# Performance work log

Measured on AMD Instinct MI355X. Metric: run time of the kernel, lower is better.

Reference implementation:

```python
import jax, jax.numpy as jnp
import numpy as np

TRANSFER_VOLUME = 0.1
KW = 1e-14  # water ion product
LN10 = float(np.log(10.0))


def binarize_weight(w):
    # clip to [-1,1], forward pass is sign(), gradient flows through the clip (STE)
    clipped = jnp.clip(w, -1.0, 1.0)
    rounded = jnp.sign(clipped)
    return clipped + jax.lax.stop_gradient(rounded - clipped)


def setup_inputs() -> dict:
    key = jax.random.key(0)
    kx, kw = jax.random.split(key)
    batch, n_in, n_out = 4096, 4096, 4096
    x = jax.random.uniform(kx, (batch, n_in), dtype=jnp.float32)
    w = jax.random.normal(kw, (n_in, n_out), dtype=jnp.float32)
    return {"x": x, "w": w}


def reference(x, w):
    binary_weights = binarize_weight(w)  # [n_in, n_out], values in {-1, 0, +1}
    input_sz = x.shape[1]
    input_h_conc = 10.0 ** (-x)                       # [B, n_in]
    input_oh_conc = KW / input_h_conc                  # [B, n_in]
    input_h_num_moles = input_h_conc * TRANSFER_VOLUME
    input_oh_num_moles = input_oh_conc * TRANSFER_VOLUME
    acid_moles_sum = input_h_num_moles @ binary_weights   # [B, n_out]
    base_moles_sum = input_oh_num_moles @ binary_weights  # [B, n_out]
    remaining_moles = acid_moles_sum - base_moles_sum
    acid_is_limiting = remaining_moles < 0
    remaining_moles_conc = jnp.abs(remaining_moles) / (input_sz * TRANSFER_VOLUME)
    resultant_h_conc = jnp.where(acid_is_limiting, KW / remaining_moles_conc, remaining_moles_conc)
    resultant_ph = -jnp.log(resultant_h_conc) / LN10
    return resultant_ph
```

## Files before the change

kernel.cpp:

```cpp
#include <hip/hip_runtime.h>
#include <math.h>

#define BATCH 4096
#define NIN   4096
#define NOUT  4096

#define BM 128
#define BN 64
#define BK 32
#define NSTAGE (NIN / BK)

typedef __attribute__((ext_vector_type(8))) short bf16x8;
typedef __attribute__((ext_vector_type(4))) float f32x4;
typedef __attribute__((ext_vector_type(8))) unsigned short u16x8;

__device__ __forceinline__ float2 compute_terms(float xv) {
    float h  = (float)exp10(-(double)xv);
    float oh = 1e-14f / h;
    return make_float2(h * 0.1f, oh * 0.1f);
}

__device__ __forceinline__ unsigned short bf16_rne(float v) {
    unsigned int b = __float_as_uint(v);
    return (unsigned short)((b + 0x7FFFu + ((b >> 16) & 1u)) >> 16);
}

__global__ __launch_bounds__(256) void precompute_terms2(const float* __restrict__ x,
                                                         float* __restrict__ a_acid,
                                                         unsigned short* __restrict__ a_b16,
                                                         int n) {
    int stride = gridDim.x * blockDim.x;
    for (int i = blockIdx.x * blockDim.x + threadIdx.x; i < n; i += stride) {
        float2 t = compute_terms(x[i]);
        a_acid[i] = t.x;
        a_b16[i]  = bf16_rne(t.y);
    }
}

__device__ __forceinline__ float signf_of(float wv) {
    return (wv > 0.f) ? 1.f : ((wv < 0.f) ? -1.f : 0.f);
}
__device__ __forceinline__ unsigned short signbf16_of(float wv) {
    return (wv > 0.f) ? 0x3F80u : ((wv < 0.f) ? 0xBF80u : 0u);
}

#define OFF_BS    16896
#define OFF_BA    25600
#define OFF_BT    35840

__global__ __launch_bounds__(256, 2) void acid_gemm_hyb(const float* __restrict__ Aa,
                                                        const unsigned short* __restrict__ Ab,
                                                        const float* __restrict__ W,
                                                        float* __restrict__ out) {
    __shared__ __align__(16) char smem[40960];
    float*          As_acid = (float*)smem;
    float*          Bs      = (float*)(smem + OFF_BS);
    unsigned short* baseA   = (unsigned short*)(smem + OFF_BA);
    unsigned short* Bt      = (unsigned short*)(smem + OFF_BT);
    float*          Bout    = (float*)smem;

    const int tid  = threadIdx.x;
    const int tx   = tid & 15;
    const int ty   = tid >> 4;
    const int lane = tid & 63;
    const int wv   = tid >> 6;
    const int g    = lane >> 4;
    const int r16  = lane & 15;
    const int bm0  = blockIdx.y * BM;
    const int bn0  = blockIdx.x * BN;

    float ma[8][4] = {}, ca[8][4] = {};
    f32x4 acc[2][4] = {};

    float4 areg[4];
    bf16x8 breg[2];
    float4 wreg[2];

    #define ISSUE_LOADS(s)                                                         \
        {                                                                          \
            const int k0_ = (s) * BK;                                              \
            _Pragma("unroll")                                                      \
            for (int r = 0; r < 4; ++r)                                            \
                areg[r] = *(const float4*)(Aa +                                    \
                    (size_t)(bm0 + (tid >> 3) + 32 * r) * NIN + k0_ + (tid & 7) * 4);\
            _Pragma("unroll")                                                      \
            for (int r = 0; r < 2; ++r)                                            \
                breg[r] = *(const bf16x8*)(Ab +                                    \
                    (size_t)(bm0 + (tid >> 2) + 64 * r) * NIN + k0_ + (tid & 3) * 8);\
            _Pragma("unroll")                                                      \
            for (int r = 0; r < 2; ++r)                                            \
                wreg[r] = *(const float4*)(W +                                     \
                    (size_t)(k0_ + (tid >> 4) + 16 * r) * NOUT + bn0 + (tid & 15) * 4);\
        }

    #define WRITE_LDS()                                                            \
        {                                                                          \
            _Pragma("unroll")                                                      \
            for (int r = 0; r < 4; ++r) {                                          \
                int m_ = (tid >> 3) + 32 * r, q_ = (tid & 7) * 4;                  \
                As_acid[(q_ + 0) * 132 + m_] = areg[r].x;                          \
                As_acid[(q_ + 1) * 132 + m_] = areg[r].y;                          \
                As_acid[(q_ + 2) * 132 + m_] = areg[r].z;                          \
                As_acid[(q_ + 3) * 132 + m_] = areg[r].w;                          \
            }                                                                      \
            _Pragma("unroll")                                                      \
            for (int r = 0; r < 2; ++r)                                            \
                *(bf16x8*)&baseA[((tid >> 2) + 64 * r) * 40 + (tid & 3) * 8] = breg[r];\
            _Pragma("unroll")                                                      \
            for (int r = 0; r < 2; ++r) {                                          \
                float4 w_ = wreg[r];                                               \
                *(float4*)&Bs[((tid >> 4) + 16 * r) * 68 + (tid & 15) * 4] =       \
                    make_float4(signf_of(w_.x), signf_of(w_.y),                    \
                                signf_of(w_.z), signf_of(w_.w));                   \
                int kk_ = (tid >> 4) + 16 * r;                                     \
                Bt[((tid & 15) * 4 + 0) * 40 + kk_] = signbf16_of(w_.x);           \
                Bt[((tid & 15) * 4 + 1) * 40 + kk_] = signbf16_of(w_.y);           \
                Bt[((tid & 15) * 4 + 2) * 40 + kk_] = signbf16_of(w_.z);           \
                Bt[((tid & 15) * 4 + 3) * 40 + kk_] = signbf16_of(w_.w);           \
            }                                                                      \
        }

    ISSUE_LOADS(0);
    WRITE_LDS();
    __syncthreads();

    for (int s = 0; s < NSTAGE; ++s) {
        if (s + 1 < NSTAGE) ISSUE_LOADS(s + 1);

        {
            bf16x8 af0 = *(const bf16x8*)&baseA[(wv * 32 +      r16) * 40 + g * 8];
            bf16x8 af1 = *(const bf16x8*)&baseA[(wv * 32 + 16 + r16) * 40 + g * 8];
            #pragma unroll
            for (int tc = 0; tc < 4; ++tc) {
                bf16x8 bf = *(const bf16x8*)&Bt[(tc * 16 + r16) * 40 + g * 8];
                acc[0][tc] = __builtin_amdgcn_mfma_f32_16x16x32_bf16(af0, bf, acc[0][tc], 0, 0, 0);
                acc[1][tc] = __builtin_amdgcn_mfma_f32_16x16x32_bf16(af1, bf, acc[1][tc], 0, 0, 0);
            }
        }

        #pragma unroll 8
        for (int k = 0; k < BK; ++k) {
            const float4 pa = *(const float4*)&As_acid[k * 132 + ty * 8];
            const float4 pb = *(const float4*)&As_acid[k * 132 + ty * 8 + 4];
            const float4 sv = *(const float4*)&Bs[k * 68 + tx * 4];
            const float av[8] = {pa.x, pa.y, pa.z, pa.w, pb.x, pb.y, pb.z, pb.w};
            const float sn[4] = {sv.x, sv.y, sv.z, sv.w};
            #pragma unroll
            for (int m = 0; m < 8; ++m)
                #pragma unroll
                for (int n = 0; n < 4; ++n)
                    ca[m][n] = fmaf(av[m], sn[n], ca[m][n]);
        }

        if (((s + 1) & 15) == 0) {
            #pragma unroll
            for (int m = 0; m < 8; ++m)
                #pragma unroll
                for (int n = 0; n < 4; ++n) {
                    ma[m][n] += ca[m][n]; ca[m][n] = 0.f;
                }
        }

        __syncthreads();
        if (s + 1 < NSTAGE) WRITE_LDS();
        __syncthreads();
    }

    #pragma unroll
    for (int tr = 0; tr < 2; ++tr)
        #pragma unroll
        for (int tc = 0; tc < 4; ++tc)
            #pragma unroll
            for (int rr = 0; rr < 4; ++rr)
                Bout[(wv * 32 + tr * 16 + g * 4 + rr) * 68 + tc * 16 + r16] = acc[tr][tc][rr];
    __syncthreads();

    #pragma unroll
    for (int m = 0; m < 8; ++m) {
        int row = ty * 8 + m;
        const float4 bv = *(const float4*)&Bout[row * 68 + tx * 4];
        const float bb[4] = {bv.x, bv.y, bv.z, bv.w};
        #pragma unroll
        for (int n = 0; n < 4; ++n) {
            float r    = ma[m][n] - bb[n];
            float conc = fabsf(r) / 409.6f;
            float hc   = (r < 0.f) ? (1e-14f / conc) : conc;
            float ph   = (-logf(hc)) / 2.302585092994046f;
            out[(size_t)(bm0 + row) * NOUT + bn0 + tx * 4 + n] = ph;
        }
    }
    #undef ISSUE_LOADS
    #undef WRITE_LDS
}

__global__ __launch_bounds__(256, 2) void acid_gemm_fly(const float* __restrict__ X,
                                                        const float* __restrict__ W,
                                                        float* __restrict__ out) {
    __shared__ float2 Asf[BK][BM + 2];
    __shared__ float  Bsf[BK][BN];
    const int tid = threadIdx.x;
    const int tx = tid & 15, ty = tid >> 4;
    const int bm0 = blockIdx.y * BM, bn0 = blockIdx.x * BN;
    float ma[8][4] = {}, mb[8][4] = {}, ca[8][4] = {}, cb[8][4] = {};
    for (int s = 0; s < NSTAGE; ++s) {
        const int k0 = s * BK;
        for (int idx = tid; idx < BM * BK; idx += 256) {
            int m = idx >> 5, k = idx & 31;
            Asf[k][m] = compute_terms(X[(size_t)(bm0 + m) * NIN + k0 + k]);
        }
        for (int idx = tid; idx < BK * BN; idx += 256) {
            int k = idx >> 6, c = idx & 63;
            Bsf[k][c] = signf_of(W[(size_t)(k0 + k) * NOUT + bn0 + c]);
        }
        __syncthreads();
        #pragma unroll 4
        for (int k = 0; k < BK; ++k) {
            float2 av[8]; float sv[4];
            #pragma unroll
            for (int m = 0; m < 8; ++m) av[m] = Asf[k][ty * 8 + m];
            #pragma unroll
            for (int n = 0; n < 4; ++n) sv[n] = Bsf[k][tx * 4 + n];
            #pragma unroll
            for (int m = 0; m < 8; ++m)
                #pragma unroll
                for (int n = 0; n < 4; ++n) {
                    ca[m][n] = fmaf(av[m].x, sv[n], ca[m][n]);
                    cb[m][n] = fmaf(av[m].y, sv[n], cb[m][n]);
                }
        }
        if (((s + 1) & 15) == 0) {
            #pragma unroll
            for (int m = 0; m < 8; ++m)
                #pragma unroll
                for (int n = 0; n < 4; ++n) {
                    ma[m][n] += ca[m][n]; ca[m][n] = 0.f;
                    mb[m][n] += cb[m][n]; cb[m][n] = 0.f;
                }
        }
        __syncthreads();
    }
    #pragma unroll
    for (int m = 0; m < 8; ++m) {
        int row = bm0 + ty * 8 + m;
        #pragma unroll
        for (int n = 0; n < 4; ++n) {
            int col = bn0 + tx * 4 + n;
            float r = ma[m][n] - mb[m][n];
            float conc = fabsf(r) / 409.6f;
            float hc = (r < 0.f) ? (1e-14f / conc) : conc;
            out[(size_t)row * NOUT + col] = (-logf(hc)) / 2.302585092994046f;
        }
    }
}

extern "C" void kernel_launch(void* const* d_in, const int* in_sizes, int n_in,
                              void* d_out, int out_size, void* d_ws, size_t ws_size,
                              hipStream_t stream) {
    const float* x = (const float*)d_in[0];
    const float* w = (const float*)d_in[1];
    float* out = (float*)d_out;

    const size_t nElem   = (size_t)BATCH * NIN;
    const size_t needWs  = nElem * 4 + nElem * 2;
    dim3 grid(NOUT / BN, BATCH / BM);

    if (ws_size >= needWs) {
        float*          a_acid = (float*)d_ws;
        unsigned short* a_b16  = (unsigned short*)((char*)d_ws + nElem * 4);
        precompute_terms2<<<4096, 256, 0, stream>>>(x, a_acid, a_b16, (int)nElem);
        acid_gemm_hyb<<<grid, dim3(256), 0, stream>>>(a_acid, a_b16, w, out);
    } else {
        acid_gemm_fly<<<grid, dim3(256), 0, stream>>>(x, w, out);
    }
}
```

Before: 2.242 ms.

## Pre-transpose acid operand and weight signs to vectorize LDS staging

The acid terms are now written by the precompute kernel in k-major (transposed) layout, and a new precompute kernel builds a transposed bf16 sign matrix of the weights. The GEMM can then store both into shared memory with vector writes instead of scattered scalar transposing stores. This removes per-tile LDS transpose work and bank-conflicting scalar stores inside the main loop. In exchange it adds an extra kernel, an extra 32 MB workspace buffer and more global reads per stage.

Measured after the change: 2.489 ms. +11.0%, slower.

```diff
diff --git a/kernel.cpp b/kernel.cpp
--- a/kernel.cpp
+++ b/kernel.cpp
@@ -11,32 +11,18 @@
 #define NSTAGE (NIN / BK)
 
 typedef __attribute__((ext_vector_type(8))) short bf16x8;
+typedef __attribute__((ext_vector_type(8))) unsigned short u16x8;
 typedef __attribute__((ext_vector_type(4))) float f32x4;
-typedef __attribute__((ext_vector_type(8))) unsigned short u16x8;
 
 __device__ __forceinline__ float2 compute_terms(float xv) {
     float h  = (float)exp10(-(double)xv);
     float oh = 1e-14f / h;
     return make_float2(h * 0.1f, oh * 0.1f);
 }
-
 __device__ __forceinline__ unsigned short bf16_rne(float v) {
     unsigned int b = __float_as_uint(v);
     return (unsigned short)((b + 0x7FFFu + ((b >> 16) & 1u)) >> 16);
 }
-
-__global__ __launch_bounds__(256) void precompute_terms2(const float* __restrict__ x,
-                                                         float* __restrict__ a_acid,
-                                                         unsigned short* __restrict__ a_b16,
-                                                         int n) {
-    int stride = gridDim.x * blockDim.x;
-    for (int i = blockIdx.x * blockDim.x + threadIdx.x; i < n; i += stride) {
-        float2 t = compute_terms(x[i]);
-        a_acid[i] = t.x;
-        a_b16[i]  = bf16_rne(t.y);
-    }
-}
-
 __device__ __forceinline__ float signf_of(float wv) {
     return (wv > 0.f) ? 1.f : ((wv < 0.f) ? -1.f : 0.f);
 }
@@ -44,12 +30,67 @@
     return (wv > 0.f) ? 0x3F80u : ((wv < 0.f) ? 0xBF80u : 0u);
 }
 
-#define OFF_BS    16896
-#define OFF_BA    25600
-#define OFF_BT    35840
-
-__global__ __launch_bounds__(256, 2) void acid_gemm_hyb(const float* __restrict__ Aa,
+__global__ __launch_bounds__(256) void precompute_A(const float* __restrict__ x,
+                                                    float* __restrict__ aaT,
+                                                    unsigned short* __restrict__ ab) {
+    __shared__ float tile[64][65];
+    const int m0 = blockIdx.y * 64, k0 = blockIdx.x * 64;
+    const int tid = threadIdx.x;
+    #pragma unroll
+    for (int it = 0; it < 4; ++it) {
+        int idx = tid + it * 256;
+        int row = idx >> 4, q = idx & 15;
+        float4 xv = *(const float4*)(x + (size_t)(m0 + row) * NIN + k0 + q * 4);
+        float2 t0 = compute_terms(xv.x), t1 = compute_terms(xv.y),
+               t2 = compute_terms(xv.z), t3 = compute_terms(xv.w);
+        *(ushort4*)(ab + (size_t)(m0 + row) * NIN + k0 + q * 4) =
+            make_ushort4(bf16_rne(t0.y), bf16_rne(t1.y), bf16_rne(t2.y), bf16_rne(t3.y));
+        tile[row][q * 4 + 0] = t0.x; tile[row][q * 4 + 1] = t1.x;
+        tile[row][q * 4 + 2] = t2.x; tile[row][q * 4 + 3] = t3.x;
+    }
+    __syncthreads();
+    #pragma unroll
+    for (int it = 0; it < 4; ++it) {
+        int idx = tid + it * 256;
+        int krow = idx >> 4, q = idx & 15;
+        float4 v = make_float4(tile[q * 4 + 0][krow], tile[q * 4 + 1][krow],
+                               tile[q * 4 + 2][krow], tile[q * 4 + 3][krow]);
+        *(float4*)(aaT + (size_t)(k0 + krow) * NIN + m0 + q * 4) = v;
+    }
+}
+
+__global__ __launch_bounds__(256) void precompute_signT(const float* __restrict__ w,
+                                                        unsigned short* __restrict__ sT) {
+    __shared__ unsigned short tile[64][68];
+    const int k0 = blockIdx.y * 64, n0 = blockIdx.x * 64;
+    const int tid = threadIdx.x;
+    #pragma unroll
+    for (int it = 0; it < 4; ++it) {
+        int idx = tid + it * 256;
+        int krow = idx >> 4, q = idx & 15;
+        float4 wv = *(const float4*)(w + (size_t)(k0 + krow) * NOUT + n0 + q * 4);
+        *(ushort4*)&tile[krow][q * 4] =
+            make_ushort4(signbf16_of(wv.x), signbf16_of(wv.y), signbf16_of(wv.z), signbf16_of(wv.w));
+    }
+    __syncthreads();
+    #pragma unroll
+    for (int it = 0; it < 2; ++it) {
+        int idx = tid + it * 256;
+        int n = idx >> 3, kc = idx & 7;
+        u16x8 v;
+        #pragma unroll
+        for (int j = 0; j < 8; ++j) v[j] = tile[kc * 8 + j][n];
+        *(u16x8*)(sT + (size_t)(n0 + n) * NIN + k0 + kc * 8) = v;
+    }
+}
+
+#define OFF_BS 16896
+#define OFF_BA 25600
+#define OFF_BT 35840
+
+__global__ __launch_bounds__(256, 2) void acid_gemm_hyb(const float* __restrict__ AaT,
                                                         const unsigned short* __restrict__ Ab,
+                                                        const unsigned short* __restrict__ SignT,
                                                         const float* __restrict__ W,
                                                         float* __restrict__ out) {
     __shared__ __align__(16) char smem[40960];
@@ -73,51 +114,45 @@
     f32x4 acc[2][4] = {};
 
     float4 areg[4];
-    bf16x8 breg[2];
+    u16x8  breg[2];
     float4 wreg[2];
+    u16x8  btreg;
 
     #define ISSUE_LOADS(s)                                                         \
         {                                                                          \
             const int k0_ = (s) * BK;                                              \
             _Pragma("unroll")                                                      \
             for (int r = 0; r < 4; ++r)                                            \
-                areg[r] = *(const float4*)(Aa +                                    \
-                    (size_t)(bm0 + (tid >> 3) + 32 * r) * NIN + k0_ + (tid & 7) * 4);\
+                areg[r] = *(const float4*)(AaT +                                   \
+                    (size_t)(k0_ + (tid >> 3)) * NIN + bm0 + ((tid & 7) + 8 * r) * 4);\
             _Pragma("unroll")                                                      \
             for (int r = 0; r < 2; ++r)                                            \
-                breg[r] = *(const bf16x8*)(Ab +                                    \
+                breg[r] = *(const u16x8*)(Ab +                                     \
                     (size_t)(bm0 + (tid >> 2) + 64 * r) * NIN + k0_ + (tid & 3) * 8);\
             _Pragma("unroll")                                                      \
             for (int r = 0; r < 2; ++r)                                            \
                 wreg[r] = *(const float4*)(W +                                     \
                     (size_t)(k0_ + (tid >> 4) + 16 * r) * NOUT + bn0 + (tid & 15) * 4);\
+            btreg = *(const u16x8*)(SignT +                                        \
+                    (size_t)(bn0 + (tid >> 2)) * NIN + k0_ + (tid & 3) * 8);       \
         }
 
     #define WRITE_LDS()                                                            \
         {                                                                          \
             _Pragma("unroll")                                                      \
-            for (int r = 0; r < 4; ++r) {                                          \
-                int m_ = (tid >> 3) + 32 * r, q_ = (tid & 7) * 4;                  \
-                As_acid[(q_ + 0) * 132 + m_] = areg[r].x;                          \
-                As_acid[(q_ + 1) * 132 + m_] = areg[r].y;                          \
-                As_acid[(q_ + 2) * 132 + m_] = areg[r].z;                          \
-                As_acid[(q_ + 3) * 132 + m_] = areg[r].w;                          \
-            }                                                                      \
+            for (int r = 0; r < 4; ++r)                                            \
+                *(float4*)&As_acid[(tid >> 3) * 132 + ((tid & 7) + 8 * r) * 4] = areg[r];\
             _Pragma("unroll")                                                      \
             for (int r = 0; r < 2; ++r)                                            \
-                *(bf16x8*)&baseA[((tid >> 2) + 64 * r) * 40 + (tid & 3) * 8] = breg[r];\
+                *(u16x8*)&baseA[((tid >> 2) + 64 * r) * 40 + (tid & 3) * 8] = breg[r];\
             _Pragma("unroll")                                                      \
             for (int r = 0; r < 2; ++r) {                                          \
                 float4 w_ = wreg[r];                                               \
                 *(float4*)&Bs[((tid >> 4) + 16 * r) * 68 + (tid & 15) * 4] =       \
                     make_float4(signf_of(w_.x), signf_of(w_.y),                    \
                                 signf_of(w_.z), signf_of(w_.w));                   \
-                int kk_ = (tid >> 4) + 16 * r;                                     \
-                Bt[((tid & 15) * 4 + 0) * 40 + kk_] = signbf16_of(w_.x);           \
-                Bt[((tid & 15) * 4 + 1) * 40 + kk_] = signbf16_of(w_.y);           \
-                Bt[((tid & 15) * 4 + 2) * 40 + kk_] = signbf16_of(w_.z);           \
-                Bt[((tid & 15) * 4 + 3) * 40 + kk_] = signbf16_of(w_.w);           \
             }                                                                      \
+            *(u16x8*)&Bt[(tid >> 2) * 40 + (tid & 3) * 8] = btreg;                 \
         }
 
     ISSUE_LOADS(0);
@@ -260,15 +295,17 @@
     const float* w = (const float*)d_in[1];
     float* out = (float*)d_out;
 
-    const size_t nElem   = (size_t)BATCH * NIN;
-    const size_t needWs  = nElem * 4 + nElem * 2;
+    const size_t nElem  = (size_t)BATCH * NIN;
+    const size_t needWs = nElem * 4 + nElem * 2 + nElem * 2;
     dim3 grid(NOUT / BN, BATCH / BM);
 
     if (ws_size >= needWs) {
-        float*          a_acid = (float*)d_ws;
-        unsigned short* a_b16  = (unsigned short*)((char*)d_ws + nElem * 4);
-        precompute_terms2<<<4096, 256, 0, stream>>>(x, a_acid, a_b16, (int)nElem);
-        acid_gemm_hyb<<<grid, dim3(256), 0, stream>>>(a_acid, a_b16, w, out);
+        float*          aaT   = (float*)d_ws;
+        unsigned short* ab    = (unsigned short*)((char*)d_ws + nElem * 4);
+        unsigned short* signT = (unsigned short*)((char*)d_ws + nElem * 6);
+        precompute_A    <<<dim3(64, 64), 256, 0, stream>>>(x, aaT, ab);
+        precompute_signT<<<dim3(64, 64), 256, 0, stream>>>(w, signT);
+        acid_gemm_hyb   <<<grid, dim3(256), 0, stream>>>(aaT, ab, signT, w, out);
     } else {
         acid_gemm_fly<<<grid, dim3(256), 0, stream>>>(x, w, out);
     }
```
